# Optimization experiments

Measured on AMD Instinct MI355X. Metric: run time of the kernel, lower is better.

Reference implementation:

```python
import jax, jax.numpy as jnp
import numpy as np

NEG_SLOPE = 0.2  # PyG GATConv default leaky_relu slope
EPS = 1e-16


def setup_inputs() -> dict:
    key = jax.random.key(0)
    ks = jax.random.split(key, 6)
    N, F, H, C, E = 50000, 128, 8, 16, 600000
    node_features = jax.random.normal(ks[0], (N, F), dtype=jnp.float32)
    edge_index = jax.random.randint(ks[1], (2, E), 0, N, dtype=jnp.int64)
    W = jax.random.normal(ks[2], (F, H * C), dtype=jnp.float32) * (1.0 / np.sqrt(F))
    att_src = jax.random.normal(ks[3], (H, C), dtype=jnp.float32)
    att_dst = jax.random.normal(ks[4], (H, C), dtype=jnp.float32)
    bias = jnp.zeros((H * C,), dtype=jnp.float32)
    return {"node_features": node_features, "edge_index": edge_index,
            "W": W, "att_src": att_src, "att_dst": att_dst, "bias": bias}


def reference(node_features, edge_index, W, att_src, att_dst, bias):
    N = node_features.shape[0]
    H, C = att_src.shape
    # Linear transform, split into heads: [N, H, C]
    x = (node_features @ W).reshape(N, H, C)
    # add self loops (PyG default add_self_loops=True)
    loop = jnp.arange(N, dtype=edge_index.dtype)
    src = jnp.concatenate([edge_index[0], loop])  # message source j
    dst = jnp.concatenate([edge_index[1], loop])  # message target i
    # per-node attention logits [N, H]
    a_src = jnp.einsum('nhc,hc->nh', x, att_src)
    a_dst = jnp.einsum('nhc,hc->nh', x, att_dst)
    # edge-wise logits with leaky relu [E, H]
    alpha = jax.nn.leaky_relu(a_src[src] + a_dst[dst], NEG_SLOPE)
    # softmax over incoming edges of each target node (segment softmax)
    amax = jax.ops.segment_max(alpha, dst, num_segments=N)
    alpha = jnp.exp(alpha - amax[dst])
    asum = jax.ops.segment_sum(alpha, dst, num_segments=N)
    alpha = alpha / (asum[dst] + EPS)
    # weighted scatter-aggregate of source features [N, H, C]
    msgs = x[src] * alpha[:, :, None]
    out = jax.ops.segment_sum(msgs, dst, num_segments=N)
    out = out.reshape(N, H * C) + bias
    # SELU activation; dropout is identity in eval mode
    return jax.nn.selu(out)
```

## Files before the change

### kernel.cpp

```cpp
#include <hip/hip_runtime.h>
#include <hip/hip_fp16.h>

#define LEAKY_SLOPE 0.2f

typedef _Float16 h8 __attribute__((ext_vector_type(8)));
typedef float f32x4 __attribute__((ext_vector_type(4)));

__device__ __forceinline__ float leaky_relu_f(float v) { return v > 0.f ? v : LEAKY_SLOPE * v; }
__device__ __forceinline__ float selu_f(float v) {
    const float sc = 1.0507009873554805f, al = 1.6732632423543772f;
    return v > 0.f ? sc * v : sc * al * expm1f(v);
}

__device__ __forceinline__ int detect_is64_wave(const int* __restrict__ e32) {
    int v = e32[2 * (threadIdx.x & 63) + 1];
    unsigned long long b = __ballot(v != 0);
    return b == 0ull ? 1 : 0;
}

__device__ __forceinline__ int edge_at(const void* edges, long long idx, int is64) {
    return is64 ? (int)((const long long*)edges)[idx] : ((const int*)edges)[idx];
}

__global__ void prep_kernel(int* __restrict__ deg, int n,
                            const float* __restrict__ W, _Float16* __restrict__ Wt,
                            int* __restrict__ state, int nstate) {
    int i = blockIdx.x * blockDim.x + threadIdx.x;
    if (i < n) deg[i] = 0;
    if (i < nstate) state[i] = 0;
    if (i < 128 * 128) {
        int k = i >> 7, c = i & 127;
        Wt[c * 128 + k] = (_Float16)W[i];
    }
}

__global__ __launch_bounds__(256) void gemmhist_kernel(
    const float* __restrict__ feats, const _Float16* __restrict__ Wt,
    const float* __restrict__ att_src, const float* __restrict__ att_dst,
    __half* __restrict__ xh, float* __restrict__ a_src, float* __restrict__ a_dst,
    int N, int gemmBlocks,
    const void* __restrict__ edges, long long E,
    int* __restrict__ deg, int* __restrict__ rank) {
    __shared__ __align__(16) _Float16 Af[64][136];
    const int t = threadIdx.x;

    if ((int)blockIdx.x >= gemmBlocks) {
        int is64 = detect_is64_wave((const int*)edges);
        long long hstride = (long long)(gridDim.x - gemmBlocks) * blockDim.x;
        for (long long e = (long long)((int)blockIdx.x - gemmBlocks) * blockDim.x + t;
             e < E; e += hstride) {
            int dst = edge_at(edges, E + e, is64);
            rank[e] = atomicAdd(&deg[dst], 1);
        }
        return;
    }

    const int bid = blockIdx.x;
    if (bid == 0) {
        if (t < 64) *(__half2*)&xh[(long long)N * 128 + 2 * t] = __floats2half2_rn(0.f, 0.f);
        if (t < 8) a_src[N * 8 + t] = -1e30f;
    }

    {
        const float4* F4 = (const float4*)feats;
#pragma unroll
        for (int i = 0; i < 8; i++) {
            int q = t + i * 256;
            int row = q >> 5;
            int c = (q & 31) * 4;
            int r_abs = bid * 64 + row;
            if (r_abs >= N) r_abs = N - 1;
            float4 v = F4[(long long)r_abs * 32 + (q & 31)];
            union { _Float16 h[4]; uint2 u; } tmp;
            tmp.h[0] = (_Float16)v.x; tmp.h[1] = (_Float16)v.y;
            tmp.h[2] = (_Float16)v.z; tmp.h[3] = (_Float16)v.w;
            *(uint2*)&Af[row][c] = tmp.u;
        }
    }
    __syncthreads();

    const int l = t & 63;
    const int w = t >> 6;
    const int lr = l & 15;
    const int lg = l >> 4;

    f32x4 acc[8];
#pragma unroll
    for (int n = 0; n < 8; n++) acc[n] = (f32x4){0.f, 0.f, 0.f, 0.f};

#pragma unroll
    for (int kk = 0; kk < 4; kk++) {
        const int k0 = kk * 32 + lg * 8;
        h8 a = *(const h8*)&Af[16 * w + lr][k0];
#pragma unroll
        for (int n = 0; n < 8; n++) {
            h8 b = *(const h8*)&Wt[(16 * n + lr) * 128 + k0];
            acc[n] = __builtin_amdgcn_mfma_f32_16x16x32_f16(a, b, acc[n], 0, 0, 0);
        }
    }

    const int rbase = bid * 64 + 16 * w + lg * 4;
#pragma unroll
    for (int n = 0; n < 8; n++) {
        float asv = att_src[n * 16 + lr];
        float adv = att_dst[n * 16 + lr];
#pragma unroll
        for (int r = 0; r < 4; r++) {
            int row_abs = rbase + r;
            float v = acc[n][r];
            if (row_abs < N) xh[(long long)row_abs * 128 + 16 * n + lr] = (__half)v;
            float ps = v * asv;
            float pd = v * adv;
            ps += __shfl_xor(ps, 1); ps += __shfl_xor(ps, 2);
            ps += __shfl_xor(ps, 4); ps += __shfl_xor(ps, 8);
            pd += __shfl_xor(pd, 1); pd += __shfl_xor(pd, 2);
            pd += __shfl_xor(pd, 4); pd += __shfl_xor(pd, 8);
            if (lr == n && row_abs < N) {
                a_src[row_abs * 8 + n] = ps;
                a_dst[row_abs * 8 + n] = pd;
            }
        }
    }
}

__global__ __launch_bounds__(256) void scanlb_kernel(const int* __restrict__ deg,
                                                     int* __restrict__ offs,
                                                     int* __restrict__ csr,
                                                     int* __restrict__ state,
                                                     int N, int nb) {
    __shared__ int lds[256];
    __shared__ int s_excl;
    const int b = blockIdx.x, t = threadIdx.x;
    const int base = b * 1024 + t * 4;

    int d[4], v[4], s = 0;
#pragma unroll
    for (int i = 0; i < 4; i++) {
        d[i] = (base + i < N) ? deg[base + i] : 0;
        v[i] = (d[i] + 7) & ~7;
        s += v[i];
    }
    lds[t] = s;
    __syncthreads();
    for (int off = 1; off < 256; off <<= 1) {
        int u = (t >= off) ? lds[t - off] : 0;
        __syncthreads();
        lds[t] += u;
        __syncthreads();
    }
    const int total = lds[255];
    const int local_excl = (t == 0) ? 0 : lds[t - 1];

    if (t == 0) {
        if (b == 0) {
            __hip_atomic_store(&state[0], (total << 2) | 2, __ATOMIC_RELEASE,
                               __HIP_MEMORY_SCOPE_AGENT);
            s_excl = 0;
        } else {
            __hip_atomic_store(&state[b], (total << 2) | 1, __ATOMIC_RELEASE,
                               __HIP_MEMORY_SCOPE_AGENT);
            int excl = 0;
            for (int j = b - 1; j >= 0; j--) {
                int st;
                do {
                    st = __hip_atomic_load(&state[j], __ATOMIC_ACQUIRE,
                                           __HIP_MEMORY_SCOPE_AGENT);
                } while ((st & 3) == 0);
                excl += st >> 2;
                if ((st & 3) == 2) break;
            }
            __hip_atomic_store(&state[b], ((excl + total) << 2) | 2, __ATOMIC_RELEASE,
                               __HIP_MEMORY_SCOPE_AGENT);
            s_excl = excl;
        }
    }
    __syncthreads();
    const int excl = s_excl;

    int run = excl + local_excl;
#pragma unroll
    for (int i = 0; i < 4; i++) {
        int idx = base + i;
        if (idx < N) {
            offs[idx] = run;
            for (int q = run + d[i]; q < run + v[i]; q++) csr[q] = N;
        }
        run += v[i];
    }
    if (b == nb - 1 && t == 255) offs[N] = excl + total;
}

__global__ void scatter_kernel(const void* __restrict__ edges, long long E,
                               const int* __restrict__ offs, const int* __restrict__ rank,
                               int* __restrict__ csr) {
    int is64 = detect_is64_wave((const int*)edges);
    long long stride = (long long)gridDim.x * blockDim.x;
    for (long long e = (long long)blockIdx.x * blockDim.x + threadIdx.x; e < E; e += stride) {
        int src = edge_at(edges, e, is64);
        int dst = edge_at(edges, E + e, is64);
        csr[offs[dst] + rank[e]] = src;
    }
}

__global__ __launch_bounds__(256) void agg_kernel(const __half* __restrict__ xh,
                                                  const float* __restrict__ a_src,
                                                  const float* __restrict__ a_dst,
                                                  const int* __restrict__ offs,
                                                  const int* __restrict__ csr,
                                                  const float* __restrict__ bias,
                                                  float* __restrict__ out, int N) {
    int node = blockIdx.x * 4 + (threadIdx.x >> 6);
    if (node >= N) return;
    int l = threadIdx.x & 63;
    int h8i = l & 7;
    int e8 = l >> 3;
    int hg = l >> 3;

    float ad_w = a_dst[node * 8 + h8i];
    float wself = expf(leaky_relu_f(a_src[node * 8 + h8i] + ad_w));
    float spart = (e8 == 0) ? wself : 0.f;

    float wself_h = __shfl(wself, hg);
    float2 xs = __half22float2(*(const __half2*)&xh[(long long)node * 128 + 2 * l]);
    float accx = wself_h * xs.x;
    float accy = wself_h * xs.y;

    int beg = offs[node], end = offs[node + 1];
    int srcv = 0;
    float w = 0.f;
    if (beg < end) {
        srcv = csr[beg + e8];
        w = expf(leaky_relu_f(a_src[srcv * 8 + h8i] + ad_w));
    }
    for (int p = beg; p < end; p += 8) {
        spart += w;
        int pn = p + 8;
        int srcv_n = 0;
        float asv_n = 0.f;
        bool more = pn < end;
        if (more) {
            srcv_n = csr[pn + e8];
            asv_n = a_src[srcv_n * 8 + h8i];
        }
        float wcur = w;
        int srcv_c = srcv;
#pragma unroll
        for (int e = 0; e < 8; e++) {
            int src = __shfl(srcv_c, e * 8);
            float we = __shfl(wcur, e * 8 + hg);
            float2 xv = __half22float2(*(const __half2*)&xh[(long long)src * 128 + 2 * l]);
            accx = fmaf(we, xv.x, accx);
            accy = fmaf(we, xv.y, accy);
        }
        w = more ? expf(leaky_relu_f(asv_n + ad_w)) : 0.f;
        srcv = srcv_n;
    }
    spart += __shfl_xor(spart, 8);
    spart += __shfl_xor(spart, 16);
    spart += __shfl_xor(spart, 32);
    float s = __shfl(spart, hg);
    float inv = 1.f / (s + 1e-16f);

    float2 b = *(const float2*)&bias[2 * l];
    float2 o;
    o.x = selu_f(fmaf(accx, inv, b.x));
    o.y = selu_f(fmaf(accy, inv, b.y));
    *(float2*)&out[(long long)node * 128 + 2 * l] = o;
}

extern "C" void kernel_launch(void* const* d_in, const int* in_sizes, int n_in,
                              void* d_out, int out_size, void* d_ws, size_t ws_size,
                              hipStream_t stream) {
    const float* feats   = (const float*)d_in[0];
    const void*  edges   = d_in[1];
    const float* W       = (const float*)d_in[2];
    const float* att_src = (const float*)d_in[3];
    const float* att_dst = (const float*)d_in[4];
    const float* bias    = (const float*)d_in[5];

    const int N = in_sizes[0] / 128;
    const long long E = in_sizes[1] / 2;
    const long long fillE = E + 7LL * N;
    float* out = (float*)d_out;

    char* ws = (char*)d_ws;
    __half*   xh    = (__half*)ws;   ws += (size_t)(N + 1) * 128 * 2;
    float*    a_src = (float*)ws;    ws += (size_t)(N + 1) * 8 * 4;
    float*    a_dst = (float*)ws;    ws += (size_t)N * 8 * 4;
    _Float16* Wt    = (_Float16*)ws; ws += 128 * 128 * 2;
    int*      deg   = (int*)ws;      ws += (size_t)N * 4;
    int*      offs  = (int*)ws;      ws += (size_t)(N + 1) * 4;
    int*      rank  = (int*)ws;      ws += (size_t)E * 4;
    int*      state = (int*)ws;      ws += 64 * 4;
    int*      csr   = (int*)ws;      ws += (size_t)fillE * 4;

    const int nb = (N + 1023) / 1024;
    const int gemmBlocks = (N + 63) / 64;
    const int histBlocks = 2048;

    prep_kernel<<<(N + 255) / 256, 256, 0, stream>>>(deg, N, W, Wt, state, nb + 1);
    gemmhist_kernel<<<gemmBlocks + histBlocks, 256, 0, stream>>>(
        feats, Wt, att_src, att_dst, xh, a_src, a_dst, N, gemmBlocks, edges, E, deg, rank);
    scanlb_kernel<<<nb, 256, 0, stream>>>(deg, offs, csr, state, N, nb);
    scatter_kernel<<<2048, 256, 0, stream>>>(edges, E, offs, rank, csr);
    agg_kernel<<<(N + 3) / 4, 256, 0, stream>>>(xh, a_src, a_dst, offs, csr, bias, out, N);
}
```

Before: 106.3 us.

## Co-schedule GEMM and histogram in same blocks; unroll aggregation by 16 edges

The GEMM+histogram kernel now launches 2048 blocks, each doing a GEMM tile (if its index is below gemmBlocks) and then a contiguous chunk of the degree histogram, instead of separate block sets. The aggregation loop processes 16 edges per iteration with two-ahead prefetching of CSR indices and attention logits, padding with the dummy node N. The intent is better overlap of the atomic histogram with the GEMM and more memory-level parallelism in the gather. It adds register pressure and changes the block count and workload balance.

```diff
diff --git a/kernel.cpp b/kernel.cpp
--- a/kernel.cpp
+++ b/kernel.cpp
@@ -43,82 +43,84 @@
     int* __restrict__ deg, int* __restrict__ rank) {
     __shared__ __align__(16) _Float16 Af[64][136];
     const int t = threadIdx.x;
-
-    if ((int)blockIdx.x >= gemmBlocks) {
+    const int bid = blockIdx.x;
+
+    if (bid < gemmBlocks) {
+        if (bid == 0) {
+            if (t < 64) *(__half2*)&xh[(long long)N * 128 + 2 * t] = __floats2half2_rn(0.f, 0.f);
+            if (t < 8) a_src[N * 8 + t] = -1e30f;
+        }
+        {
+            const float4* F4 = (const float4*)feats;
+#pragma unroll
+            for (int i = 0; i < 8; i++) {
+                int q = t + i * 256;
+                int row = q >> 5;
+                int c = (q & 31) * 4;
+                int r_abs = bid * 64 + row;
+                if (r_abs >= N) r_abs = N - 1;
+                float4 v = F4[(long long)r_abs * 32 + (q & 31)];
+                union { _Float16 h[4]; uint2 u; } tmp;
+                tmp.h[0] = (_Float16)v.x; tmp.h[1] = (_Float16)v.y;
+                tmp.h[2] = (_Float16)v.z; tmp.h[3] = (_Float16)v.w;
+                *(uint2*)&Af[row][c] = tmp.u;
+            }
+        }
+        __syncthreads();
+
+        const int l = t & 63;
+        const int w = t >> 6;
+        const int lr = l & 15;
+        const int lg = l >> 4;
+
+        f32x4 acc[8];
+#pragma unroll
+        for (int n = 0; n < 8; n++) acc[n] = (f32x4){0.f, 0.f, 0.f, 0.f};
+
+#pragma unroll
+        for (int kk = 0; kk < 4; kk++) {
+            const int k0 = kk * 32 + lg * 8;
+            h8 a = *(const h8*)&Af[16 * w + lr][k0];
+#pragma unroll
+            for (int n = 0; n < 8; n++) {
+                h8 b = *(const h8*)&Wt[(16 * n + lr) * 128 + k0];
+                acc[n] = __builtin_amdgcn_mfma_f32_16x16x32_f16(a, b, acc[n], 0, 0, 0);
+            }
+        }
+
+        const int rbase = bid * 64 + 16 * w + lg * 4;
+#pragma unroll
+        for (int n = 0; n < 8; n++) {
+            float asv = att_src[n * 16 + lr];
+            float adv = att_dst[n * 16 + lr];
+#pragma unroll
+            for (int r = 0; r < 4; r++) {
+                int row_abs = rbase + r;
+                float v = acc[n][r];
+                if (row_abs < N) xh[(long long)row_abs * 128 + 16 * n + lr] = (__half)v;
+                float ps = v * asv;
+                float pd = v * adv;
+                ps += __shfl_xor(ps, 1); ps += __shfl_xor(ps, 2);
+                ps += __shfl_xor(ps, 4); ps += __shfl_xor(ps, 8);
+                pd += __shfl_xor(pd, 1); pd += __shfl_xor(pd, 2);
+                pd += __shfl_xor(pd, 4); pd += __shfl_xor(pd, 8);
+                if (lr == n && row_abs < N) {
+                    a_src[row_abs * 8 + n] = ps;
+                    a_dst[row_abs * 8 + n] = pd;
+                }
+            }
+        }
+    }
+
+    {
         int is64 = detect_is64_wave((const int*)edges);
-        long long hstride = (long long)(gridDim.x - gemmBlocks) * blockDim.x;
-        for (long long e = (long long)((int)blockIdx.x - gemmBlocks) * blockDim.x + t;
-             e < E; e += hstride) {
+        long long per = (E + (long long)gridDim.x - 1) / gridDim.x;
+        long long s0 = (long long)bid * per;
+        long long s1 = s0 + per;
+        if (s1 > E) s1 = E;
+        for (long long e = s0 + t; e < s1; e += 256) {
             int dst = edge_at(edges, E + e, is64);
             rank[e] = atomicAdd(&deg[dst], 1);
-        }
-        return;
-    }
-
-    const int bid = blockIdx.x;
-    if (bid == 0) {
-        if (t < 64) *(__half2*)&xh[(long long)N * 128 + 2 * t] = __floats2half2_rn(0.f, 0.f);
-        if (t < 8) a_src[N * 8 + t] = -1e30f;
-    }
-
-    {
-        const float4* F4 = (const float4*)feats;
-#pragma unroll
-        for (int i = 0; i < 8; i++) {
-            int q = t + i * 256;
-            int row = q >> 5;
-            int c = (q & 31) * 4;
-            int r_abs = bid * 64 + row;
-            if (r_abs >= N) r_abs = N - 1;
-            float4 v = F4[(long long)r_abs * 32 + (q & 31)];
-            union { _Float16 h[4]; uint2 u; } tmp;
-            tmp.h[0] = (_Float16)v.x; tmp.h[1] = (_Float16)v.y;
-            tmp.h[2] = (_Float16)v.z; tmp.h[3] = (_Float16)v.w;
-            *(uint2*)&Af[row][c] = tmp.u;
-        }
-    }
-    __syncthreads();
-
-    const int l = t & 63;
-    const int w = t >> 6;
-    const int lr = l & 15;
-    const int lg = l >> 4;
-
-    f32x4 acc[8];
-#pragma unroll
-    for (int n = 0; n < 8; n++) acc[n] = (f32x4){0.f, 0.f, 0.f, 0.f};
-
-#pragma unroll
-    for (int kk = 0; kk < 4; kk++) {
-        const int k0 = kk * 32 + lg * 8;
-        h8 a = *(const h8*)&Af[16 * w + lr][k0];
-#pragma unroll
-        for (int n = 0; n < 8; n++) {
-            h8 b = *(const h8*)&Wt[(16 * n + lr) * 128 + k0];
-            acc[n] = __builtin_amdgcn_mfma_f32_16x16x32_f16(a, b, acc[n], 0, 0, 0);
-        }
-    }
-
-    const int rbase = bid * 64 + 16 * w + lg * 4;
-#pragma unroll
-    for (int n = 0; n < 8; n++) {
-        float asv = att_src[n * 16 + lr];
-        float adv = att_dst[n * 16 + lr];
-#pragma unroll
-        for (int r = 0; r < 4; r++) {
-            int row_abs = rbase + r;
-            float v = acc[n][r];
-            if (row_abs < N) xh[(long long)row_abs * 128 + 16 * n + lr] = (__half)v;
-            float ps = v * asv;
-            float pd = v * adv;
-            ps += __shfl_xor(ps, 1); ps += __shfl_xor(ps, 2);
-            ps += __shfl_xor(ps, 4); ps += __shfl_xor(ps, 8);
-            pd += __shfl_xor(pd, 1); pd += __shfl_xor(pd, 2);
-            pd += __shfl_xor(pd, 4); pd += __shfl_xor(pd, 8);
-            if (lr == n && row_abs < N) {
-                a_src[row_abs * 8 + n] = ps;
-                a_dst[row_abs * 8 + n] = pd;
-            }
         }
     }
 }
@@ -226,35 +228,51 @@
     float accy = wself_h * xs.y;
 
     int beg = offs[node], end = offs[node + 1];
-    int srcv = 0;
-    float w = 0.f;
+    int srcvA = N, srcvB = N;
+    float wA = 0.f, asvB = -1e30f;
     if (beg < end) {
-        srcv = csr[beg + e8];
-        w = expf(leaky_relu_f(a_src[srcv * 8 + h8i] + ad_w));
-    }
-    for (int p = beg; p < end; p += 8) {
-        spart += w;
-        int pn = p + 8;
-        int srcv_n = 0;
-        float asv_n = 0.f;
-        bool more = pn < end;
-        if (more) {
-            srcv_n = csr[pn + e8];
-            asv_n = a_src[srcv_n * 8 + h8i];
-        }
-        float wcur = w;
-        int srcv_c = srcv;
+        srcvA = csr[beg + e8];
+        wA = expf(leaky_relu_f(a_src[srcvA * 8 + h8i] + ad_w));
+    }
+    if (beg + 8 < end) {
+        srcvB = csr[beg + 8 + e8];
+        asvB = a_src[srcvB * 8 + h8i];
+    }
+
+    for (int p = beg; p < end; p += 16) {
+        bool hasB = (p + 8) < end;
+        float wB = hasB ? expf(leaky_relu_f(asvB + ad_w)) : 0.f;
+        spart += wA + wB;
+
+        int srcvC = N, srcvD = N;
+        float asvC = -1e30f, asvD = -1e30f;
+        bool hasC = (p + 16) < end, hasD = (p + 24) < end;
+        if (hasC) { srcvC = csr[p + 16 + e8]; asvC = a_src[srcvC * 8 + h8i]; }
+        if (hasD) { srcvD = csr[p + 24 + e8]; asvD = a_src[srcvD * 8 + h8i]; }
+
 #pragma unroll
         for (int e = 0; e < 8; e++) {
-            int src = __shfl(srcv_c, e * 8);
-            float we = __shfl(wcur, e * 8 + hg);
+            int src = __shfl(srcvA, e * 8);
+            float we = __shfl(wA, e * 8 + hg);
             float2 xv = __half22float2(*(const __half2*)&xh[(long long)src * 128 + 2 * l]);
             accx = fmaf(we, xv.x, accx);
             accy = fmaf(we, xv.y, accy);
         }
-        w = more ? expf(leaky_relu_f(asv_n + ad_w)) : 0.f;
-        srcv = srcv_n;
-    }
+#pragma unroll
+        for (int e = 0; e < 8; e++) {
+            int src = __shfl(srcvB, e * 8);
+            float we = __shfl(wB, e * 8 + hg);
+            float2 xv = __half22float2(*(const __half2*)&xh[(long long)src * 128 + 2 * l]);
+            accx = fmaf(we, xv.x, accx);
+            accy = fmaf(we, xv.y, accy);
+        }
+
+        wA = hasC ? expf(leaky_relu_f(asvC + ad_w)) : 0.f;
+        srcvA = srcvC;
+        srcvB = srcvD;
+        asvB = asvD;
+    }
+
     spart += __shfl_xor(spart, 8);
     spart += __shfl_xor(spart, 16);
     spart += __shfl_xor(spart, 32);
@@ -296,10 +314,10 @@
 
     const int nb = (N + 1023) / 1024;
     const int gemmBlocks = (N + 63) / 64;
-    const int histBlocks = 2048;
+    const int packBlocks = 2048;
 
     prep_kernel<<<(N + 255) / 256, 256, 0, stream>>>(deg, N, W, Wt, state, nb + 1);
-    gemmhist_kernel<<<gemmBlocks + histBlocks, 256, 0, stream>>>(
+    gemmhist_kernel<<<packBlocks, 256, 0, stream>>>(
         feats, Wt, att_src, att_dst, xh, a_src, a_dst, N, gemmBlocks, edges, E, deg, rank);
     scanlb_kernel<<<nb, 256, 0, stream>>>(deg, offs, csr, state, N, nb);
     scatter_kernel<<<2048, 256, 0, stream>>>(edges, E, offs, rank, csr);
```

Result: slower. 109.7 us (+3.2%).
